# Kernel optimization log

Measured on AMD Instinct MI355X. Metric: run time of the kernel, lower is better.

Reference implementation:

```python
import jax, jax.numpy as jnp
import numpy as np

# --- problem-size constants (uniform instance of the ragged structure) ---
B = 64            # claims
EVI = 5           # evidence sequences per claim
SEQS = B * EVI    # total PLM sequences
L = 256           # tokens per sequence
D = 768           # in_channels (PLM hidden)
WORDS = 32        # word-nodes per evidence
TPW = 4           # token refs averaged per word (word_select mean)
N = B * EVI * WORDS   # total graph nodes = 10240
E = N * 16            # edges
R = 4                 # num_relations
DOUT = 768            # out_channels
LH = 1024             # linear_hidden_channels
NC = 3                # num_class


def setup_inputs() -> dict:
    key = jax.random.key(0)
    ks = jax.random.split(key, 16)
    s = 0.02
    return {
        "token_feats": jax.random.normal(ks[0], (SEQS, L, D), jnp.float32),
        "concat_cls": jax.random.normal(ks[1], (B, D), jnp.float32),
        "W_rel1": jax.random.normal(ks[2], (R, D, D), jnp.float32) * s,
        "W_root1": jax.random.normal(ks[3], (D, D), jnp.float32) * s,
        "b1": jnp.zeros((D,), jnp.float32),
        "W_rel2": jax.random.normal(ks[4], (R, D, DOUT), jnp.float32) * s,
        "W_root2": jax.random.normal(ks[5], (D, DOUT), jnp.float32) * s,
        "b2": jnp.zeros((DOUT,), jnp.float32),
        "att_w0": jax.random.normal(ks[6], (D + 2 * DOUT, DOUT), jnp.float32) * s,
        "att_w1": jax.random.normal(ks[7], (DOUT, 1), jnp.float32) * s,
        "lin1_w": jax.random.normal(ks[8], (2 * DOUT + D, LH), jnp.float32) * s,
        "lin1_b": jnp.zeros((LH,), jnp.float32),
        "lin2_w": jax.random.normal(ks[9], (LH, NC), jnp.float32) * s,
        "lin2_b": jnp.zeros((NC,), jnp.float32),
        "word_token_idx": jax.random.randint(ks[10], (N * TPW,), 0, SEQS * L),
        "edge_index": jax.random.randint(ks[11], (2, E), 0, N),
        "edge_type": jax.random.randint(ks[12], (E,), 0, R),
        "claim_seq_idx": jnp.arange(B) * EVI,  # first sequence of each claim
    }


def _rgcn(x, edge_index, edge_type, W_rel, W_root, b):
    # PyG RGCNConv with mean aggregation per relation + root transform + bias
    xr = jnp.einsum('nd,rde->rne', x, W_rel)        # [R, N, Dout]
    src, dst = edge_index[0], edge_index[1]
    msg = xr[edge_type, src]                        # [E, Dout]
    seg = dst * R + edge_type                       # (target, relation) buckets
    cnt = jax.ops.segment_sum(jnp.ones((E,), x.dtype), seg, num_segments=N * R)
    msg = msg / jnp.maximum(cnt, 1.0)[seg][:, None]
    agg = jax.ops.segment_sum(msg, dst, num_segments=N)
    return agg + x @ W_root + b


def reference(token_feats, concat_cls, W_rel1, W_root1, b1, W_rel2, W_root2, b2,
              att_w0, att_w1, lin1_w, lin1_b, lin2_w, lin2_b,
              word_token_idx, edge_index, edge_type, claim_seq_idx):
    # word_select: mean of token vectors per word-node (TPW uniform here)
    tok = token_feats.reshape(-1, D)
    x = tok[word_token_idx].reshape(N, TPW, D).mean(axis=1)       # [N, D]
    claim_cls = token_feats[claim_seq_idx, 0, :]                  # [B, D]

    # 2 RGCN layers with ReLU
    x = jax.nn.relu(_rgcn(x, edge_index, edge_type, W_rel1, W_root1, b1))
    x = jax.nn.relu(_rgcn(x, edge_index, edge_type, W_rel2, W_root2, b2))

    # per-evidence mean||max pooling over its words (uniform WORDS per evidence)
    xe = x.reshape(B * EVI, WORDS, DOUT)
    ev = jnp.concatenate([xe.mean(axis=1), xe.max(axis=1)], axis=-1)  # [B*EVI, 2*Dout]

    # attention scores per evidence, conditioned on the claim CLS
    cc = jnp.repeat(claim_cls, EVI, axis=0)                       # [B*EVI, D]
    h = jax.nn.relu(jnp.concatenate([cc, ev], axis=-1) @ att_w0)
    p = h @ att_w1                                                # [B*EVI, 1]

    # per-claim softmax over its evidences, weighted sum of evidence reps
    a = jax.nn.softmax(p.reshape(B, EVI), axis=1)
    graph = jnp.einsum('be,bed->bd', a, ev.reshape(B, EVI, 2 * DOUT))  # [B, 2*Dout]

    rep = jnp.concatenate([graph, concat_cls], axis=-1)           # [B, 2*Dout + D]
    # dropout is identity in eval mode
    out = jax.nn.log_softmax(jax.nn.relu(rep @ lin1_w + lin1_b) @ lin2_w + lin2_b, axis=-1)
    attention = jax.nn.sigmoid(p[:, 0])                           # [B*EVI]
    return out, attention
```

## Files before the change

kernel.cpp:

```cpp
#include <hip/hip_runtime.h>
#include <hip/hip_fp16.h>


#define BN 64
#define EVI 5
#define SEQS (BN * EVI)
#define LSEQ 256
#define DIM 768
#define WORDS 32
#define TPW 4
#define NNODE (BN * EVI * WORDS)
#define NEDGE (NNODE * 16)
#define RREL 4
#define DOUT 768
#define LH 1024
#define NCLS 3
#define KBIG (5 * DIM)
#define KATT (DIM + 2 * DOUT)

typedef float f32x4 __attribute__((ext_vector_type(4)));
typedef __bf16 bf16x8 __attribute__((ext_vector_type(8)));

__device__ inline unsigned short f2bf(float f) {
    union { float f; unsigned int u; } v; v.f = f;
    unsigned int u = v.u;
    unsigned int lsb = (u >> 16) & 1u;
    u += 0x7fffu + lsb;
    return (unsigned short)(u >> 16);
}
__device__ inline float bf2f(unsigned short h) {
    union { float f; unsigned int u; } v; v.u = ((unsigned int)h) << 16; return v.f;
}

__device__ inline float ldin(const void* p, long i, int f) {
    if (f == 1) return __half2float(((const __half*)p)[i]);
    if (f == 2) return bf2f(((const unsigned short*)p)[i]);
    return ((const float*)p)[i];
}

__global__ void detect_kernel(const void* w, int* flag) {
    const int lane = threadIdx.x;
    const unsigned int* u32 = (const unsigned int*)w;
    const unsigned short* u16 = (const unsigned short*)w;
    int tiny = 0;
    for (int i = lane; i < 2048; i += 64) {
        unsigned int b = u32[i];
        float f; __builtin_memcpy(&f, &b, 4);
        float a = fabsf(f);
        if (!(a > 1e-10f)) tiny++;
    }
    int band = 0;
    for (int i = lane; i < 4096; i += 64) {
        unsigned short h = u16[i];
        int e8 = (h >> 7) & 0xFF;
        if (h == 0 || (e8 >= 0x66 && e8 <= 0x86)) band++;
    }
#pragma unroll
    for (int o = 32; o > 0; o >>= 1) {
        tiny += __shfl_down(tiny, o);
        band += __shfl_down(band, o);
    }
    if (lane == 0) {
        if (tiny > 1024) { *flag = 1; return; }
        *flag = (band > 3900) ? 2 : 0;
    }
}

__global__ void convert_kernel(const void* __restrict__ src, float* __restrict__ dst,
                               long n, const int* __restrict__ flag)
{
    int f = *flag;
    long stride = (long)gridDim.x * 256;
    for (long i = (long)blockIdx.x * 256 + threadIdx.x; i < n; i += stride)
        dst[i] = ldin(src, i, f);
}

__global__ __launch_bounds__(256) void gather_mean_kernel(
    const void* __restrict__ tok, const int* __restrict__ widx,
    unsigned short* __restrict__ xb, const int* __restrict__ flag)
{
    int f = *flag;
    int n = blockIdx.x;
    long i0 = widx[n * 4 + 0], i1 = widx[n * 4 + 1];
    long i2 = widx[n * 4 + 2], i3 = widx[n * 4 + 3];
    for (int c = threadIdx.x; c < DIM; c += 256) {
        float s = ldin(tok, i0 * DIM + c, f) + ldin(tok, i1 * DIM + c, f)
                + ldin(tok, i2 * DIM + c, f) + ldin(tok, i3 * DIM + c, f);
        xb[(long)n * DIM + c] = f2bf(s * 0.25f);
    }
}

__global__ void count_kernel(const int* __restrict__ ei, const int* __restrict__ et,
                             int* __restrict__ cnt)
{
    int e = blockIdx.x * 256 + threadIdx.x;
    if (e >= NEDGE) return;
    int dst = ei[NEDGE + e];
    int r = et[e];
    atomicAdd(&cnt[dst * RREL + r], 1);
}

__global__ __launch_bounds__(1024) void scan_kernel(const int* __restrict__ cnt,
                                                    int* __restrict__ offs, int n)
{
    const int CH = (n + 1023) >> 10;
    int tid = threadIdx.x;
    int base = tid * CH;
    int s = 0;
    for (int i = 0; i < CH; i++)
        if (base + i < n) s += cnt[base + i];
    __shared__ int buf[1024];
    buf[tid] = s;
    __syncthreads();
    for (int o = 1; o < 1024; o <<= 1) {
        int t = (tid >= o) ? buf[tid - o] : 0;
        __syncthreads();
        buf[tid] += t;
        __syncthreads();
    }
    int run = (tid == 0) ? 0 : buf[tid - 1];
    if (tid == 0) offs[0] = 0;
    for (int i = 0; i < CH; i++) {
        if (base + i < n) {
            run += cnt[base + i];
            offs[base + i + 1] = run;
        }
    }
}

__global__ void fill_kernel(const int* __restrict__ ei, const int* __restrict__ et,
                            const int* __restrict__ offs, int* __restrict__ cursor,
                            int* __restrict__ sorted)
{
    int e = blockIdx.x * 256 + threadIdx.x;
    if (e >= NEDGE) return;
    int src = ei[e];
    int dst = ei[NEDGE + e];
    int r = et[e];
    int seg = dst * RREL + r;
    int pos = offs[seg] + atomicAdd(&cursor[seg], 1);
    sorted[pos] = src;
}

__global__ __launch_bounds__(256) void aggregate_kernel(
    const unsigned short* __restrict__ xsrc, long xstride,
    const int* __restrict__ offs, const int* __restrict__ sorted,
    unsigned short* __restrict__ A, int write_root)
{
    int n = blockIdx.x;
    long base = (long)n * KBIG;
    for (int r = 0; r < RREL; r++) {
        int s0 = offs[n * RREL + r], s1 = offs[n * RREL + r + 1];
        float inv = 1.0f / (float)max(s1 - s0, 1);
        for (int c = threadIdx.x; c < DIM; c += 256) {
            float acc = 0.0f;
            for (int i = s0; i < s1; i++) {
                long s = sorted[i];
                acc += bf2f(xsrc[s * xstride + c]);
            }
            A[base + r * DIM + c] = f2bf(acc * inv);
        }
    }
    if (write_root) {
        for (int c = threadIdx.x; c < DIM; c += 256)
            A[base + 4 * DIM + c] = xsrc[(long)n * xstride + c];
    }
}

__global__ __launch_bounds__(256) void transpose_cast_kernel(
    const void* __restrict__ in, int Ncols,
    unsigned short* __restrict__ out, int outStride, int colOff,
    const int* __restrict__ flag)
{
    int f = *flag;
    __shared__ float t[32][33];
    int kt = blockIdx.x * 32, nt = blockIdx.y * 32;
    int lx = threadIdx.x & 31, ly = threadIdx.x >> 5;
    for (int i = 0; i < 4; i++)
        t[ly + i * 8][lx] = ldin(in, (long)(kt + ly + i * 8) * Ncols + nt + lx, f);
    __syncthreads();
    for (int i = 0; i < 4; i++)
        out[(long)(nt + ly + i * 8) * outStride + colOff + kt + lx] = f2bf(t[lx][ly + i * 8]);
}

__global__ __launch_bounds__(256) void gemm_bt_kernel(
    const unsigned short* __restrict__ A, const unsigned short* __restrict__ Bt,
    int K, const float* __restrict__ bias, int relu,
    float* __restrict__ outF, long strideF,
    unsigned short* __restrict__ outB, long strideB)
{
    __shared__ __align__(16) unsigned short As[128 * 32];
    __shared__ __align__(16) unsigned short Bs[128 * 32];
    const int tid = threadIdx.x;
    const int lane = tid & 63, wv = tid >> 6;
    const int wr = wv >> 1, wc = wv & 1;
    const int lr = lane & 15, q = lane >> 4;
    const long m0 = (long)blockIdx.x * 128, n0 = (long)blockIdx.y * 128;

    f32x4 acc[4][4] = {};

    for (int kt = 0; kt < K; kt += 32) {
#pragma unroll
        for (int i = 0; i < 2; i++) {
            int chunk = i * 256 + tid;
            int row = chunk >> 2, kc = (chunk & 3) * 8;
            const unsigned short* ga = A + (m0 + row) * K + kt + kc;
            const unsigned short* gb = Bt + (n0 + row) * K + kt + kc;
            int ldsbase = (i * 256 + wv * 64) * 8;
            __builtin_amdgcn_global_load_lds(
                (const __attribute__((address_space(1))) void*)ga,
                (__attribute__((address_space(3))) void*)&As[ldsbase], 16, 0, 0);
            __builtin_amdgcn_global_load_lds(
                (const __attribute__((address_space(1))) void*)gb,
                (__attribute__((address_space(3))) void*)&Bs[ldsbase], 16, 0, 0);
        }
        __syncthreads();
        bf16x8 af[4], bfr[4];
#pragma unroll
        for (int i = 0; i < 4; i++)
            af[i] = *(const bf16x8*)&As[(wr * 64 + i * 16 + lr) * 32 + q * 8];
#pragma unroll
        for (int j = 0; j < 4; j++)
            bfr[j] = *(const bf16x8*)&Bs[(wc * 64 + j * 16 + lr) * 32 + q * 8];
#pragma unroll
        for (int i = 0; i < 4; i++)
#pragma unroll
            for (int j = 0; j < 4; j++)
                acc[i][j] = __builtin_amdgcn_mfma_f32_16x16x32_bf16(af[i], bfr[j], acc[i][j], 0, 0, 0);
        __syncthreads();
    }

#pragma unroll
    for (int i = 0; i < 4; i++) {
#pragma unroll
        for (int j = 0; j < 4; j++) {
            long col = n0 + wc * 64 + j * 16 + lr;
            float bv = bias ? bias[col] : 0.0f;
#pragma unroll
            for (int r = 0; r < 4; r++) {
                long row = m0 + wr * 64 + i * 16 + q * 4 + r;
                float v = acc[i][j][r] + bv;
                if (relu) v = fmaxf(v, 0.0f);
                if (outF) outF[row * strideF + col] = v;
                if (outB) outB[row * strideB + col] = f2bf(v);
            }
        }
    }
}

__global__ __launch_bounds__(256) void pool_cc_kernel(
    const float* __restrict__ C2, const void* __restrict__ tok,
    const int* __restrict__ csi, unsigned short* __restrict__ A3,
    float* __restrict__ evF, const int* __restrict__ flag)
{
    int f = *flag;
    int s = blockIdx.x;
    int b = s / EVI;
    long seq = csi[b];
    for (int c = threadIdx.x; c < DIM; c += 256) {
        float mx = -1e30f, sm = 0.0f;
        const float* col = C2 + (long)s * WORDS * DOUT + c;
        for (int w = 0; w < WORDS; w++) {
            float v = col[(long)w * DOUT];
            sm += v;
            mx = fmaxf(mx, v);
        }
        float mean = sm * (1.0f / WORDS);
        evF[(long)s * (2 * DOUT) + c] = mean;
        evF[(long)s * (2 * DOUT) + DOUT + c] = mx;
        A3[(long)s * KATT + c] = f2bf(ldin(tok, seq * LSEQ * DIM + c, f));
        A3[(long)s * KATT + DIM + c] = f2bf(mean);
        A3[(long)s * KATT + DIM + DOUT + c] = f2bf(mx);
    }
}

__global__ __launch_bounds__(256) void pdot_kernel(
    const float* __restrict__ h, const void* __restrict__ w1, float* __restrict__ p,
    const int* __restrict__ flag)
{
    int f = *flag;
    int i = blockIdx.x;
    float s = 0.0f;
    for (int k = threadIdx.x; k < DOUT; k += 256) s += h[(long)i * DOUT + k] * ldin(w1, k, f);
    __shared__ float red[256];
    red[threadIdx.x] = s;
    __syncthreads();
    for (int o = 128; o > 0; o >>= 1) {
        if (threadIdx.x < o) red[threadIdx.x] += red[threadIdx.x + o];
        __syncthreads();
    }
    if (threadIdx.x == 0) p[i] = red[0];
}

__global__ void att_out_kernel(const float* __restrict__ p, float* __restrict__ out)
{
    int i = blockIdx.x * 256 + threadIdx.x;
    if (i < SEQS) out[BN * NCLS + i] = 1.0f / (1.0f + __expf(-p[i]));
}

__global__ __launch_bounds__(256) void softgraph_kernel(
    const float* __restrict__ p, const float* __restrict__ evF,
    const void* __restrict__ ccls, unsigned short* __restrict__ A4,
    const int* __restrict__ flag)
{
    int f = *flag;
    int b = blockIdx.x;
    __shared__ float a[EVI];
    if (threadIdx.x == 0) {
        float m = -1e30f;
        for (int e = 0; e < EVI; e++) m = fmaxf(m, p[b * EVI + e]);
        float s = 0.0f, ex[EVI];
        for (int e = 0; e < EVI; e++) { ex[e] = __expf(p[b * EVI + e] - m); s += ex[e]; }
        for (int e = 0; e < EVI; e++) a[e] = ex[e] / s;
    }
    __syncthreads();
    for (int d = threadIdx.x; d < 2 * DOUT; d += 256) {
        float g = 0.0f;
        for (int e = 0; e < EVI; e++)
            g += a[e] * evF[(long)(b * EVI + e) * (2 * DOUT) + d];
        A4[(long)b * KATT + d] = f2bf(g);
    }
    for (int c = threadIdx.x; c < DIM; c += 256)
        A4[(long)b * KATT + 2 * DOUT + c] = f2bf(ldin(ccls, (long)b * DIM + c, f));
}

__global__ __launch_bounds__(256) void final_kernel(
    const float* __restrict__ C4, const void* __restrict__ w2,
    const void* __restrict__ bb, float* __restrict__ out,
    const int* __restrict__ flag)
{
    int f = *flag;
    int b = blockIdx.x;
    float s0 = 0.0f, s1 = 0.0f, s2 = 0.0f;
    for (int k = threadIdx.x; k < LH; k += 256) {
        float h = C4[(long)b * LH + k];
        s0 += h * ldin(w2, k * NCLS + 0, f);
        s1 += h * ldin(w2, k * NCLS + 1, f);
        s2 += h * ldin(w2, k * NCLS + 2, f);
    }
    __shared__ float r0[256], r1[256], r2[256];
    int t = threadIdx.x;
    r0[t] = s0; r1[t] = s1; r2[t] = s2;
    __syncthreads();
    for (int o = 128; o > 0; o >>= 1) {
        if (t < o) { r0[t] += r0[t + o]; r1[t] += r1[t + o]; r2[t] += r2[t + o]; }
        __syncthreads();
    }
    if (t == 0) {
        float l0 = r0[0] + ldin(bb, 0, f), l1 = r1[0] + ldin(bb, 1, f), l2 = r2[0] + ldin(bb, 2, f);
        float m = fmaxf(l0, fmaxf(l1, l2));
        float lse = logf(__expf(l0 - m) + __expf(l1 - m) + __expf(l2 - m)) + m;
        out[b * NCLS + 0] = l0 - lse;
        out[b * NCLS + 1] = l1 - lse;
        out[b * NCLS + 2] = l2 - lse;
    }
}

extern "C" void kernel_launch(void* const* d_in, const int* in_sizes, int n_in,
                              void* d_out, int out_size, void* d_ws, size_t ws_size,
                              hipStream_t stream)
{
    const void* tok      = d_in[0];
    const void* ccls_r   = d_in[1];
    const void* W_rel1_r = d_in[2];
    const void* W_root1_r= d_in[3];
    const void* b1_r     = d_in[4];
    const void* W_rel2_r = d_in[5];
    const void* W_root2_r= d_in[6];
    const void* b2_r     = d_in[7];
    const void* att_w0_r = d_in[8];
    const void* att_w1_r = d_in[9];
    const void* lin1_w_r = d_in[10];
    const void* lin1_b_r = d_in[11];
    const void* lin2_w_r = d_in[12];
    const void* lin2_b_r = d_in[13];
    const int* widx      = (const int*)d_in[14];
    const int* ei        = (const int*)d_in[15];
    const int* et        = (const int*)d_in[16];
    const int* csi       = (const int*)d_in[17];
    float* out           = (float*)d_out;

    char* ws = (char*)d_ws;
    size_t off = 0;
    auto alloc = [&](size_t bytes) { size_t o = off; off = (off + bytes + 255) & ~(size_t)255; return o; };

    int* flag   = (int*)(ws + alloc(256));
    float* b1F     = (float*)(ws + alloc((size_t)DIM * 4));
    float* b2F     = (float*)(ws + alloc((size_t)DOUT * 4));
    float* l1bF    = (float*)(ws + alloc((size_t)LH * 4));
    unsigned short* xb  = (unsigned short*)(ws + alloc((size_t)NNODE * DIM * 2));
    unsigned short* A1  = (unsigned short*)(ws + alloc((size_t)NNODE * KBIG * 2));
    unsigned short* X1  = (unsigned short*)(ws + alloc((size_t)NNODE * DOUT * 2));
    unsigned short* Wt1 = (unsigned short*)(ws + alloc((size_t)DIM * KBIG * 2));
    unsigned short* Wt2 = (unsigned short*)(ws + alloc((size_t)DIM * KBIG * 2));
    unsigned short* Wt3 = (unsigned short*)(ws + alloc((size_t)DOUT * KATT * 2));
    unsigned short* Wt4 = (unsigned short*)(ws + alloc((size_t)LH * KATT * 2));
    float* C2           = (float*)(ws + alloc((size_t)NNODE * DOUT * 4));
    unsigned short* A3  = (unsigned short*)(ws + alloc((size_t)384 * KATT * 2));
    float* C3           = (float*)(ws + alloc((size_t)384 * DOUT * 4));
    float* evF          = (float*)(ws + alloc((size_t)SEQS * 2 * DOUT * 4));
    float* pbuf         = (float*)(ws + alloc((size_t)SEQS * 4));
    unsigned short* A4  = (unsigned short*)(ws + alloc((size_t)128 * KATT * 2));
    float* C4           = (float*)(ws + alloc((size_t)128 * LH * 4));
    int* cnt            = (int*)(ws + alloc((size_t)2 * NNODE * RREL * 4));
    int* cursor         = cnt + NNODE * RREL;
    int* offs           = (int*)(ws + alloc((size_t)(NNODE * RREL + 1) * 4));
    int* sorted         = (int*)(ws + alloc((size_t)NEDGE * 4));
    (void)ws_size; (void)in_sizes; (void)n_in; (void)out_size;

    detect_kernel<<<1, 64, 0, stream>>>(W_rel1_r, flag);
    auto conv = [&](const void* src, float* dst, long n) {
        int grid = (int)min((n + 255) / 256, (long)2048);
        convert_kernel<<<grid, 256, 0, stream>>>(src, dst, n, flag);
    };
    conv(b1_r,     b1F,     DIM);
    conv(b2_r,     b2F,     DOUT);
    conv(lin1_b_r, l1bF,    LH);

    hipMemsetAsync(cnt, 0, (size_t)2 * NNODE * RREL * 4, stream);
    count_kernel<<<NEDGE / 256, 256, 0, stream>>>(ei, et, cnt);
    scan_kernel<<<1, 1024, 0, stream>>>(cnt, offs, NNODE * RREL);
    fill_kernel<<<NEDGE / 256, 256, 0, stream>>>(ei, et, offs, cursor, sorted);

    gather_mean_kernel<<<NNODE, 256, 0, stream>>>(tok, widx, xb, flag);

    transpose_cast_kernel<<<dim3(96, 24), 256, 0, stream>>>(W_rel1_r, DIM, Wt1, KBIG, 0, flag);
    transpose_cast_kernel<<<dim3(24, 24), 256, 0, stream>>>(W_root1_r, DIM, Wt1, KBIG, 4 * DIM, flag);
    transpose_cast_kernel<<<dim3(96, 24), 256, 0, stream>>>(W_rel2_r, DOUT, Wt2, KBIG, 0, flag);
    transpose_cast_kernel<<<dim3(24, 24), 256, 0, stream>>>(W_root2_r, DOUT, Wt2, KBIG, 4 * DIM, flag);
    transpose_cast_kernel<<<dim3(72, 24), 256, 0, stream>>>(att_w0_r, DOUT, Wt3, KATT, 0, flag);
    transpose_cast_kernel<<<dim3(72, 32), 256, 0, stream>>>(lin1_w_r, LH, Wt4, KATT, 0, flag);

    aggregate_kernel<<<NNODE, 256, 0, stream>>>(xb, DIM, offs, sorted, A1, 1);
    gemm_bt_kernel<<<dim3(NNODE / 128, DIM / 128), 256, 0, stream>>>(
        A1, Wt1, KBIG, b1F, 1, nullptr, 0, X1, DOUT);

    aggregate_kernel<<<NNODE, 256, 0, stream>>>(X1, DOUT, offs, sorted, A1, 1);
    gemm_bt_kernel<<<dim3(NNODE / 128, DOUT / 128), 256, 0, stream>>>(
        A1, Wt2, KBIG, b2F, 1, C2, DOUT, nullptr, 0);

    pool_cc_kernel<<<SEQS, 256, 0, stream>>>(C2, tok, csi, A3, evF, flag);
    gemm_bt_kernel<<<dim3(3, DOUT / 128), 256, 0, stream>>>(
        A3, Wt3, KATT, nullptr, 1, C3, DOUT, nullptr, 0);
    pdot_kernel<<<SEQS, 256, 0, stream>>>(C3, att_w1_r, pbuf, flag);
    att_out_kernel<<<(SEQS + 255) / 256, 256, 0, stream>>>(pbuf, out);
    softgraph_kernel<<<BN, 256, 0, stream>>>(pbuf, evF, ccls_r, A4, flag);

    gemm_bt_kernel<<<dim3(1, LH / 128), 256, 0, stream>>>(
        A4, Wt4, KATT, l1bF, 1, C4, LH, nullptr, 0);
    final_kernel<<<BN, 256, 0, stream>>>(C4, lin2_w_r, lin2_b_r, out, flag);
}
```

Before: 1.058 ms.

## Vectorize RGCN aggregation with per-relation thread groups and fuse attention tail kernels

The aggregate kernel now uses 768 threads per node, split into four groups of 192, one per relation. Each thread loads 4 bf16 values at a time and unrolls the edge loop by four with independent accumulators, which replaces the serial per-relation scalar loop. The pdot, sigmoid and softgraph kernels are merged into one per-claim kernel, removing two launches and the pbuf round trip. Larger blocks may limit occupancy, and the fused kernel runs only 64 blocks that do serial reductions.

```diff
diff --git a/kernel.cpp b/kernel.cpp
--- a/kernel.cpp
+++ b/kernel.cpp
@@ -20,6 +20,7 @@
 
 typedef float f32x4 __attribute__((ext_vector_type(4)));
 typedef __bf16 bf16x8 __attribute__((ext_vector_type(8)));
+typedef unsigned short u16x4 __attribute__((ext_vector_type(4)));
 
 __device__ inline unsigned short f2bf(float f) {
     union { float f; unsigned int u; } v; v.f = f;
@@ -142,29 +143,50 @@
     sorted[pos] = src;
 }
 
-__global__ __launch_bounds__(256) void aggregate_kernel(
+__global__ __launch_bounds__(768) void aggregate_kernel(
     const unsigned short* __restrict__ xsrc, long xstride,
     const int* __restrict__ offs, const int* __restrict__ sorted,
     unsigned short* __restrict__ A, int write_root)
 {
-    int n = blockIdx.x;
-    long base = (long)n * KBIG;
-    for (int r = 0; r < RREL; r++) {
-        int s0 = offs[n * RREL + r], s1 = offs[n * RREL + r + 1];
-        float inv = 1.0f / (float)max(s1 - s0, 1);
-        for (int c = threadIdx.x; c < DIM; c += 256) {
-            float acc = 0.0f;
-            for (int i = s0; i < s1; i++) {
-                long s = sorted[i];
-                acc += bf2f(xsrc[s * xstride + c]);
-            }
-            A[base + r * DIM + c] = f2bf(acc * inv);
-        }
-    }
-    if (write_root) {
-        for (int c = threadIdx.x; c < DIM; c += 256)
-            A[base + 4 * DIM + c] = xsrc[(long)n * xstride + c];
-    }
+    const int n = blockIdx.x;
+    const int t = threadIdx.x;
+    const int g = t / 192;
+    const int l = t - g * 192;
+    const long rs4 = xstride >> 2;
+    const u16x4* __restrict__ xs4 = (const u16x4*)xsrc;
+    u16x4* __restrict__ Ap = (u16x4*)A;
+    const long baseQ = ((long)n * KBIG) >> 2;
+    const int s0 = offs[n * RREL + g];
+    const int s1 = offs[n * RREL + g + 1];
+    const float inv = 1.0f / (float)max(s1 - s0, 1);
+    float p0[4] = {0, 0, 0, 0}, p1[4] = {0, 0, 0, 0};
+    float p2[4] = {0, 0, 0, 0}, p3[4] = {0, 0, 0, 0};
+    int i = s0;
+    for (; i + 3 < s1; i += 4) {
+        int e0 = sorted[i], e1 = sorted[i + 1], e2 = sorted[i + 2], e3 = sorted[i + 3];
+        u16x4 w0 = xs4[(long)e0 * rs4 + l];
+        u16x4 w1 = xs4[(long)e1 * rs4 + l];
+        u16x4 w2 = xs4[(long)e2 * rs4 + l];
+        u16x4 w3 = xs4[(long)e3 * rs4 + l];
+#pragma unroll
+        for (int c = 0; c < 4; c++) {
+            p0[c] += bf2f(w0[c]); p1[c] += bf2f(w1[c]);
+            p2[c] += bf2f(w2[c]); p3[c] += bf2f(w3[c]);
+        }
+    }
+    for (; i < s1; i++) {
+        int e = sorted[i];
+        u16x4 w = xs4[(long)e * rs4 + l];
+#pragma unroll
+        for (int c = 0; c < 4; c++) p0[c] += bf2f(w[c]);
+    }
+    u16x4 o;
+#pragma unroll
+    for (int c = 0; c < 4; c++)
+        o[c] = f2bf(((p0[c] + p1[c]) + (p2[c] + p3[c])) * inv);
+    Ap[baseQ + g * (DIM / 4) + l] = o;
+    if (write_root && t < 192)
+        Ap[baseQ + RREL * (DIM / 4) + t] = xs4[(long)n * rs4 + t];
 }
 
 __global__ __launch_bounds__(256) void transpose_cast_kernel(
@@ -274,53 +296,48 @@
     }
 }
 
-__global__ __launch_bounds__(256) void pdot_kernel(
-    const float* __restrict__ h, const void* __restrict__ w1, float* __restrict__ p,
+__global__ __launch_bounds__(256) void att_finish_kernel(
+    const float* __restrict__ C3, const void* __restrict__ w1,
+    const float* __restrict__ evF, const void* __restrict__ ccls,
+    float* __restrict__ out, unsigned short* __restrict__ A4,
     const int* __restrict__ flag)
 {
     int f = *flag;
-    int i = blockIdx.x;
-    float s = 0.0f;
-    for (int k = threadIdx.x; k < DOUT; k += 256) s += h[(long)i * DOUT + k] * ldin(w1, k, f);
+    int b = blockIdx.x;
+    int t = threadIdx.x;
     __shared__ float red[256];
-    red[threadIdx.x] = s;
+    __shared__ float a[EVI];
+    __shared__ float psh[EVI];
+    for (int e = 0; e < EVI; e++) {
+        int s = b * EVI + e;
+        float sum = 0.0f;
+        for (int k = t; k < DOUT; k += 256)
+            sum += C3[(long)s * DOUT + k] * ldin(w1, k, f);
+        red[t] = sum;
+        __syncthreads();
+        for (int o = 128; o > 0; o >>= 1) {
+            if (t < o) red[t] += red[t + o];
+            __syncthreads();
+        }
+        if (t == 0) psh[e] = red[0];
+        __syncthreads();
+    }
+    if (t < EVI) out[BN * NCLS + b * EVI + t] = 1.0f / (1.0f + __expf(-psh[t]));
+    if (t == 0) {
+        float m = -1e30f;
+        for (int e = 0; e < EVI; e++) m = fmaxf(m, psh[e]);
+        float ssum = 0.0f, ex[EVI];
+        for (int e = 0; e < EVI; e++) { ex[e] = __expf(psh[e] - m); ssum += ex[e]; }
+        for (int e = 0; e < EVI; e++) a[e] = ex[e] / ssum;
+    }
     __syncthreads();
-    for (int o = 128; o > 0; o >>= 1) {
-        if (threadIdx.x < o) red[threadIdx.x] += red[threadIdx.x + o];
-        __syncthreads();
-    }
-    if (threadIdx.x == 0) p[i] = red[0];
-}
-
-__global__ void att_out_kernel(const float* __restrict__ p, float* __restrict__ out)
-{
-    int i = blockIdx.x * 256 + threadIdx.x;
-    if (i < SEQS) out[BN * NCLS + i] = 1.0f / (1.0f + __expf(-p[i]));
-}
-
-__global__ __launch_bounds__(256) void softgraph_kernel(
-    const float* __restrict__ p, const float* __restrict__ evF,
-    const void* __restrict__ ccls, unsigned short* __restrict__ A4,
-    const int* __restrict__ flag)
-{
-    int f = *flag;
-    int b = blockIdx.x;
-    __shared__ float a[EVI];
-    if (threadIdx.x == 0) {
-        float m = -1e30f;
-        for (int e = 0; e < EVI; e++) m = fmaxf(m, p[b * EVI + e]);
-        float s = 0.0f, ex[EVI];
-        for (int e = 0; e < EVI; e++) { ex[e] = __expf(p[b * EVI + e] - m); s += ex[e]; }
-        for (int e = 0; e < EVI; e++) a[e] = ex[e] / s;
-    }
-    __syncthreads();
-    for (int d = threadIdx.x; d < 2 * DOUT; d += 256) {
-        float g = 0.0f;
+    for (int d = t; d < 2 * DOUT; d += 256) {
+        float gg = 0.0f;
         for (int e = 0; e < EVI; e++)
-            g += a[e] * evF[(long)(b * EVI + e) * (2 * DOUT) + d];
-        A4[(long)b * KATT + d] = f2bf(g);
-    }
-    for (int c = threadIdx.x; c < DIM; c += 256)
+            gg += a[e] * evF[(long)(b * EVI + e) * (2 * DOUT) + d];
+        A4[(long)b * KATT + d] = f2bf(gg);
+    }
+    for (int c = t; c < DIM; c += 256)
         A4[(long)b * KATT + 2 * DOUT + c] = f2bf(ldin(ccls, (long)b * DIM + c, f));
 }
 
@@ -399,7 +416,6 @@
     unsigned short* A3  = (unsigned short*)(ws + alloc((size_t)384 * KATT * 2));
     float* C3           = (float*)(ws + alloc((size_t)384 * DOUT * 4));
     float* evF          = (float*)(ws + alloc((size_t)SEQS * 2 * DOUT * 4));
-    float* pbuf         = (float*)(ws + alloc((size_t)SEQS * 4));
     unsigned short* A4  = (unsigned short*)(ws + alloc((size_t)128 * KATT * 2));
     float* C4           = (float*)(ws + alloc((size_t)128 * LH * 4));
     int* cnt            = (int*)(ws + alloc((size_t)2 * NNODE * RREL * 4));
@@ -431,20 +447,18 @@
     transpose_cast_kernel<<<dim3(72, 24), 256, 0, stream>>>(att_w0_r, DOUT, Wt3, KATT, 0, flag);
     transpose_cast_kernel<<<dim3(72, 32), 256, 0, stream>>>(lin1_w_r, LH, Wt4, KATT, 0, flag);
 
-    aggregate_kernel<<<NNODE, 256, 0, stream>>>(xb, DIM, offs, sorted, A1, 1);
+    aggregate_kernel<<<NNODE, 768, 0, stream>>>(xb, DIM, offs, sorted, A1, 1);
     gemm_bt_kernel<<<dim3(NNODE / 128, DIM / 128), 256, 0, stream>>>(
         A1, Wt1, KBIG, b1F, 1, nullptr, 0, X1, DOUT);
 
-    aggregate_kernel<<<NNODE, 256, 0, stream>>>(X1, DOUT, offs, sorted, A1, 1);
+    aggregate_kernel<<<NNODE, 768, 0, stream>>>(X1, DOUT, offs, sorted, A1, 1);
     gemm_bt_kernel<<<dim3(NNODE / 128, DOUT / 128), 256, 0, stream>>>(
         A1, Wt2, KBIG, b2F, 1, C2, DOUT, nullptr, 0);
 
     pool_cc_kernel<<<SEQS, 256, 0, stream>>>(C2, tok, csi, A3, evF, flag);
     gemm_bt_kernel<<<dim3(3, DOUT / 128), 256, 0, stream>>>(
         A3, Wt3, KATT, nullptr, 1, C3, DOUT, nullptr, 0);
-    pdot_kernel<<<SEQS, 256, 0, stream>>>(C3, att_w1_r, pbuf, flag);
-    att_out_kernel<<<(SEQS + 255) / 256, 256, 0, stream>>>(pbuf, out);
-    softgraph_kernel<<<BN, 256, 0, stream>>>(pbuf, evF, ccls_r, A4, flag);
+    att_finish_kernel<<<BN, 256, 0, stream>>>(C3, att_w1_r, evF, ccls_r, out, A4, flag);
 
     gemm_bt_kernel<<<dim3(1, LH / 128), 256, 0, stream>>>(
         A4, Wt4, KATT, l1bF, 1, C4, LH, nullptr, 0);
```

Result: faster. 950.0 us (-10.2%).
